# Kernel tuning notes

Hardware: AMD Instinct MI355X
Metric: run time of the kernel (lower is better)

The kernel has to match this reference:

```python
import jax, jax.numpy as jnp
import numpy as np

H = 128      # hidden_size
L = 2        # num_layers
IN0 = 96     # seq_feature_size + context_feature_size
OUT = 1

def _xavier(k, shape):
    fan_out, fan_in = shape
    lim = (6.0 / (fan_in + fan_out)) ** 0.5
    return jax.random.uniform(k, shape, jnp.float32, -lim, lim)

def _orth(k, n):
    q, _ = jnp.linalg.qr(jax.random.normal(k, (n, n)))
    return q.astype(jnp.float32)

def setup_inputs() -> dict:
    key = jax.random.key(0)
    ks = jax.random.split(key, 16)
    B, S, F_seq, F_ctx = 512, 512, 64, 32
    inp = {
        "seq_features": jax.random.normal(ks[0], (B, S, F_seq), jnp.float32),
        "context_features": jax.random.normal(ks[1], (B, F_ctx), jnp.float32),
    }
    for i in range(L):
        in_size = IN0 if i == 0 else H
        inp[f"tau{i}"] = jax.random.normal(ks[2 + 5 * i], (H,), jnp.float32) * 0.1
        inp[f"Win{i}"] = _xavier(ks[3 + 5 * i], (H, in_size))
        inp[f"Wrec{i}"] = _orth(ks[4 + 5 * i], H)
        inp[f"Wg{i}"] = _xavier(ks[5 + 5 * i], (H, in_size + H))
        inp[f"bg{i}"] = jnp.zeros((H,), jnp.float32)
    inp["W1"] = _xavier(ks[12], (H // 2, H))
    inp["b1"] = jnp.zeros((H // 2,), jnp.float32)
    inp["W2"] = _xavier(ks[13], (OUT, H // 2))
    inp["b2"] = jnp.zeros((OUT,), jnp.float32)
    return inp

def _cell_step(x, h, tau_p, Win, Wrec, Wg, bg):
    # LTC cell: RK4 integration of dh/dt = -h/tau + W_in x + gate * W_rec h
    tau = jax.nn.softplus(tau_p) + 1.0
    def rhs(hh):
        gate = jax.nn.sigmoid(jnp.tanh(jnp.concatenate([x, hh], axis=-1) @ Wg.T + bg))
        return -hh / tau + x @ Win.T + gate * (hh @ Wrec.T)
    k1 = rhs(h)
    k2 = rhs(h + 0.5 * k1)
    k3 = rhs(h + 0.5 * k2)
    k4 = rhs(h + k3)
    return jnp.tanh(h + (k1 + 2.0 * k2 + 2.0 * k3 + k4) / 6.0)

def reference(seq_features, context_features, tau0, Win0, Wrec0, Wg0, bg0,
              tau1, Win1, Wrec1, Wg1, bg1, W1, b1, W2, b2):
    B, S, _ = seq_features.shape
    ctx = jnp.broadcast_to(context_features[:, None, :], (B, S, context_features.shape[-1]))
    x = jnp.concatenate([seq_features, ctx], axis=-1)     # [B,S,IN0]
    xs = jnp.swapaxes(x, 0, 1)                            # [S,B,IN0] time-major
    cells = [(tau0, Win0, Wrec0, Wg0, bg0), (tau1, Win1, Wrec1, Wg1, bg1)]
    h_init = tuple(jnp.zeros((B, H), x.dtype) for _ in range(L))

    def step(hs, xt):
        new = []
        inp = xt
        for hi, p in zip(hs, cells):
            hn = _cell_step(inp, hi, *p)
            new.append(hn)
            inp = hn
        return tuple(new), None

    hs, _ = jax.lax.scan(step, h_init, xs)
    h_last = hs[-1]                                       # [B,H]
    # classifier (dropout is identity in eval mode)
    out = jax.nn.sigmoid(jax.nn.relu(h_last @ W1.T + b1) @ W2.T + b2)
    return out.reshape(B, -1)
```

## Files before the change

### kernel.cpp

```cpp
#include <hip/hip_runtime.h>


typedef _Float16 f16;
typedef _Float16 f16x4 __attribute__((ext_vector_type(4)));
typedef _Float16 f16x8 __attribute__((ext_vector_type(8)));
typedef float f32x4 __attribute__((ext_vector_type(4)));

#define NSTEP 512
#define OFF_A0 0
#define OFF_A1 32768
#define OFF_AIO 65536
#define OFF_AX 98304
#define W_TOTAL 122880

#define HQ0 0
#define HQ1 4352
#define L0A 8704
#define L0B 13056
#define L1A 17408
#define L1B 21760
#define L1H 26112
#define XT 30464

__device__ __forceinline__ float rcp_f(float x) { return __builtin_amdgcn_rcpf(x); }
__device__ __forceinline__ float tanh_f(float x) {
  float e = __expf(2.f * x);
  return 1.f - 2.f * rcp_f(e + 1.f);
}
__device__ __forceinline__ float sig_poly(float t) {
  float s = t * t;
  float p = fmaf(s, 2.1356861e-5f, -2.1081349e-4f);
  p = fmaf(s, p, 2.0833333e-3f);
  p = fmaf(s, p, -2.0833333e-2f);
  p = fmaf(s, p, 0.25f);
  return fmaf(t, p, 0.5f);
}

__global__ __launch_bounds__(256) void prep_kernel(
    const float* __restrict__ Win0, const float* __restrict__ Wrec0,
    const float* __restrict__ Wg0, const float* __restrict__ Win1,
    const float* __restrict__ Wrec1, const float* __restrict__ Wg1,
    f16* __restrict__ W) {
  int i = blockIdx.x * 256 + threadIdx.x;
  if (i >= W_TOTAL) return;
  if (i < OFF_AX) {
    int sec = i >> 15;
    int r = i & 32767;
    int j = r & 7, lane = (r >> 3) & 63, kc = (r >> 9) & 3, sel = (r >> 11) & 1,
        w = (r >> 12) & 7;
    int row = w * 16 + (lane & 15);
    int k = kc * 32 + ((lane >> 4) << 3) + j;
    float v;
    if (sec == 0)
      v = sel ? Wrec0[row * 128 + k] : Wg0[row * 224 + 96 + k];
    else if (sec == 1)
      v = sel ? Wrec1[row * 128 + k] : Wg1[row * 256 + 128 + k];
    else
      v = sel ? Wg1[row * 256 + k] : Win1[row * 128 + k];
    W[i] = (f16)v;
  } else {
    int r = i - OFF_AX;
    int j = r & 7, lane = (r >> 3) & 63, g = r >> 9;
    int kc = g % 3, sg = g / 3;
    int sel = sg & 1, w = sg >> 1;
    int row = w * 16 + (lane & 15);
    int k = kc * 32 + ((lane >> 4) << 3) + j;
    W[i] = (f16)(sel ? Wg0[row * 224 + k] : Win0[row * 96 + k]);
  }
}

#define MFMA16(A, B, C) __builtin_amdgcn_mfma_f32_16x16x32_f16((A), (B), (C), 0, 0, 0)
#define ZERO4 ((f32x4){0.f, 0.f, 0.f, 0.f})

#define MM2(SRC)                                                    \
  {                                                                 \
    const f16* bp_ = (SRC) + c * 136 + 8 * q;                       \
    _Pragma("unroll") for (int kc_ = 0; kc_ < 4; ++kc_) {           \
      f16x8 bf_ = *(const f16x8*)(bp_ + kc_ * 32);                  \
      ga[0] = MFMA16(awg[0][kc_], bf_, ga[0]);                      \
      ra[0] = MFMA16(awr[0][kc_], bf_, ra[0]);                      \
      ga[1] = MFMA16(awg[1][kc_], bf_, ga[1]);                      \
      ra[1] = MFMA16(awr[1][kc_], bf_, ra[1]);                      \
    }                                                               \
  }

#define MMIO(SRC, KCN)                                              \
  {                                                                 \
    const f16* bp_ = (SRC) + c * 136 + 8 * q;                       \
    _Pragma("unroll") for (int kc_ = 0; kc_ < (KCN); ++kc_) {       \
      f16x8 bf_ = *(const f16x8*)(bp_ + kc_ * 32);                  \
      ga[0] = MFMA16(au[0][kc_], bf_, ga[0]);                       \
      ra[0] = MFMA16(ag2[0][kc_], bf_, ra[0]);                      \
      ga[1] = MFMA16(au[1][kc_], bf_, ga[1]);                       \
      ra[1] = MFMA16(ag2[1][kc_], bf_, ra[1]);                      \
    }                                                               \
  }

#define GATEALL(WC, HC, DST)                                        \
  _Pragma("unroll") for (int i2_ = 0; i2_ < 2; ++i2_) {             \
    f16x4 hv_;                                                      \
    _Pragma("unroll") for (int r_ = 0; r_ < 4; ++r_) {              \
      float th_ = tanh_f(ga[i2_][r_] + gx[i2_][r_]);                \
      float gt_ = sig_poly(th_);                                    \
      float kk_ = fmaf(gt_, ra[i2_][r_],                            \
                       fmaf(-itv[i2_][r_], hhc[i2_][r_], u[i2_][r_])); \
      ksum[i2_][r_] = fmaf((WC), kk_, ksum[i2_][r_]);               \
      float hn_ = fmaf((HC), kk_, hst[i2_][r_]);                    \
      hhc[i2_][r_] = hn_;                                           \
      hv_[r_] = (f16)hn_;                                           \
    }                                                               \
    *(f16x4*)((DST) + c * 136 + jb[i2_]) = hv_;                     \
  }

#define GATEFIN(DST)                                                \
  _Pragma("unroll") for (int i2_ = 0; i2_ < 2; ++i2_) {             \
    f16x4 hv_;                                                      \
    _Pragma("unroll") for (int r_ = 0; r_ < 4; ++r_) {              \
      float th_ = tanh_f(ga[i2_][r_] + gx[i2_][r_]);                \
      float gt_ = sig_poly(th_);                                    \
      float kk_ = fmaf(gt_, ra[i2_][r_],                            \
                       fmaf(-itv[i2_][r_], hhc[i2_][r_], u[i2_][r_])); \
      float ks_ = ksum[i2_][r_] + kk_;                              \
      float hn_ = tanh_f(fmaf(ks_, 0.16666667f, hst[i2_][r_]));     \
      hst[i2_][r_] = hn_;                                           \
      hhc[i2_][r_] = hn_;                                           \
      hv_[r_] = (f16)hn_;                                           \
    }                                                               \
    *(f16x4*)((DST) + c * 136 + jb[i2_]) = hv_;                     \
  }

#define ZACC { ga[0] = ZERO4; ra[0] = ZERO4; ga[1] = ZERO4; ra[1] = ZERO4; }

__global__ __launch_bounds__(512, 2) void ltc_kernel(
    const float* __restrict__ seq, const float* __restrict__ ctx,
    const float* __restrict__ tau0p, const float* __restrict__ bg0p,
    const float* __restrict__ tau1p, const float* __restrict__ bg1p,
    const float* __restrict__ W1, const float* __restrict__ b1,
    const float* __restrict__ W2, const float* __restrict__ b2,
    const f16* __restrict__ W, float* __restrict__ out) {
  __shared__ __align__(16) char smem[32768];
  f16* hq0 = (f16*)(smem + HQ0);
  f16* hq1 = (f16*)(smem + HQ1);
  f16* l0a = (f16*)(smem + L0A);
  f16* l0b = (f16*)(smem + L0B);
  f16* l1a = (f16*)(smem + L1A);
  f16* l1b = (f16*)(smem + L1B);
  f16* l1h = (f16*)(smem + L1H);
  f16* xt = (f16*)(smem + XT);

  const int tid = threadIdx.x;
  const int w8 = tid >> 6, lane = tid & 63;
  const int q = lane >> 4, c = lane & 15;
  const int wl = w8 & 3;
  const bool isL0 = (w8 < 4);
  const int bg = blockIdx.x;
  int jb[2];
  jb[0] = 32 * wl + 4 * q;
  jb[1] = jb[0] + 16;

  f16* bufA = isL0 ? l0a : l1a;
  f16* bufB = isL0 ? l0b : l1b;

  f16x8 awg[2][4], awr[2][4], au[2][4], ag2[2][4];
  f16x8 bctx;
  if (isL0) {
#pragma unroll
    for (int i2 = 0; i2 < 2; ++i2) {
      int T = 2 * wl + i2;
#pragma unroll
      for (int kc = 0; kc < 4; ++kc) {
        awg[i2][kc] = *(const f16x8*)(W + OFF_A0 + (((T * 2 + 0) * 4 + kc) * 64 + lane) * 8);
        awr[i2][kc] = *(const f16x8*)(W + OFF_A0 + (((T * 2 + 1) * 4 + kc) * 64 + lane) * 8);
      }
#pragma unroll
      for (int kc = 0; kc < 3; ++kc) {
        au[i2][kc] = *(const f16x8*)(W + OFF_AX + (((T * 2 + 0) * 3 + kc) * 64 + lane) * 8);
        ag2[i2][kc] = *(const f16x8*)(W + OFF_AX + (((T * 2 + 1) * 3 + kc) * 64 + lane) * 8);
      }
      au[i2][3] = (f16x8)(f16)0.f;
      ag2[i2][3] = (f16x8)(f16)0.f;
    }
    const float* cp = ctx + (bg * 16 + c) * 32 + 8 * q;
#pragma unroll
    for (int j = 0; j < 8; ++j) bctx[j] = (f16)cp[j];
  } else {
#pragma unroll
    for (int i2 = 0; i2 < 2; ++i2) {
      int T = 2 * wl + i2;
#pragma unroll
      for (int kc = 0; kc < 4; ++kc) {
        awg[i2][kc] = *(const f16x8*)(W + OFF_A1 + (((T * 2 + 0) * 4 + kc) * 64 + lane) * 8);
        awr[i2][kc] = *(const f16x8*)(W + OFF_A1 + (((T * 2 + 1) * 4 + kc) * 64 + lane) * 8);
        au[i2][kc] = *(const f16x8*)(W + OFF_AIO + (((T * 2 + 0) * 4 + kc) * 64 + lane) * 8);
        ag2[i2][kc] = *(const f16x8*)(W + OFF_AIO + (((T * 2 + 1) * 4 + kc) * 64 + lane) * 8);
      }
    }
  }

  const float* taup = isL0 ? tau0p : tau1p;
  const float* bgp = isL0 ? bg0p : bg1p;
  f32x4 itv[2], bgv[2];
#pragma unroll
  for (int i2 = 0; i2 < 2; ++i2)
#pragma unroll
    for (int r = 0; r < 4; ++r) {
      float t = taup[jb[i2] + r];
      itv[i2][r] = 1.f / (logf(1.f + __expf(t)) + 1.f);
      bgv[i2][r] = bgp[jb[i2] + r];
    }

  f32x4 hst[2], hhc[2], u[2], gx[2], ksum[2], ga[2], ra[2];
  hst[0] = hst[1] = hhc[0] = hhc[1] = ZERO4;
  ksum[0] = ksum[1] = ZERO4;

  for (int j = tid; j < 2176; j += 512) {
    hq1[j] = (f16)0.f;
    l1h[j] = (f16)0.f;
  }
  const int bs = tid >> 4, fp = tid & 15;
  const size_t seqrow = ((size_t)(bg * 16 + bs)) * NSTEP * 64 + 4 * fp;
  if (tid < 256) {
    float4 sv = *(const float4*)(seq + seqrow);
    *(f16x4*)(xt + bs * 72 + 4 * fp) =
        (f16x4){(f16)sv.x, (f16)sv.y, (f16)sv.z, (f16)sv.w};
  }
  __syncthreads();

  float4 sqv = {0.f, 0.f, 0.f, 0.f};

#pragma unroll 1
  for (int i = 0; i <= NSTEP; ++i) {
    const f16* hprev = ((i + 1) & 1) ? hq1 : hq0;

    if (isL0) {
      if (i < NSTEP) {
        if (i + 1 < NSTEP) sqv = *(const float4*)(seq + seqrow + (size_t)(i + 1) * 64);
        ZACC;
        {
          f16x8 bx0 = *(const f16x8*)(xt + c * 72 + 8 * q);
          f16x8 bx1 = *(const f16x8*)(xt + c * 72 + 32 + 8 * q);
#pragma unroll
          for (int i2 = 0; i2 < 2; ++i2) {
            ga[i2] = MFMA16(au[i2][0], bx0, ga[i2]);
            ra[i2] = MFMA16(ag2[i2][0], bx0, ra[i2]);
            ga[i2] = MFMA16(au[i2][1], bx1, ga[i2]);
            ra[i2] = MFMA16(ag2[i2][1], bx1, ra[i2]);
            ga[i2] = MFMA16(au[i2][2], bctx, ga[i2]);
            ra[i2] = MFMA16(ag2[i2][2], bctx, ra[i2]);
          }
        }
#pragma unroll
        for (int i2 = 0; i2 < 2; ++i2) {
          u[i2] = ga[i2];
#pragma unroll
          for (int r = 0; r < 4; ++r) gx[i2][r] = ra[i2][r] + bgv[i2][r];
        }
        ZACC;
        MM2(hprev);
        ksum[0] = ZERO4; ksum[1] = ZERO4;
        GATEALL(1.0f, 0.5f, bufA);
      }
    } else {
      if (i >= 1) {
        ZACC;
        MMIO(hprev, 4);
#pragma unroll
        for (int i2 = 0; i2 < 2; ++i2) {
          u[i2] = ga[i2];
#pragma unroll
          for (int r = 0; r < 4; ++r) gx[i2][r] = ra[i2][r] + bgv[i2][r];
        }
        ZACC;
        MM2(l1h);
        ksum[0] = ZERO4; ksum[1] = ZERO4;
        GATEALL(1.0f, 0.5f, bufA);
      }
    }
    __syncthreads();

    if ((isL0 && i < NSTEP) || (!isL0 && i >= 1)) {
      ZACC;
      MM2(bufA);
      GATEALL(2.0f, 0.5f, bufB);
    }
    __syncthreads();

    if ((isL0 && i < NSTEP) || (!isL0 && i >= 1)) {
      ZACC;
      MM2(bufB);
      GATEALL(2.0f, 1.0f, bufA);
    }
    __syncthreads();

    if (isL0) {
      if (i < NSTEP) {
        ZACC;
        MM2(bufA);
        GATEFIN((i & 1) ? hq1 : hq0);
        if (tid < 256 && i + 1 < NSTEP)
          *(f16x4*)(xt + bs * 72 + 4 * fp) =
              (f16x4){(f16)sqv.x, (f16)sqv.y, (f16)sqv.z, (f16)sqv.w};
      }
    } else {
      if (i >= 1) {
        ZACC;
        MM2(bufA);
        GATEFIN(l1h);
      }
    }
    __syncthreads();
  }

  float* h1f = (float*)smem;
  if (!isL0) {
#pragma unroll
    for (int i2 = 0; i2 < 2; ++i2)
      *(f32x4*)(h1f + c * 132 + jb[i2]) = hst[i2];
  }
  __syncthreads();
  float* z1 = (float*)(smem + 16 * 132 * 4);
  {
    int b = tid >> 5, o = tid & 31;
#pragma unroll
    for (int hlf = 0; hlf < 2; ++hlf) {
      int oo = o + 32 * hlf;
      const float* wr = W1 + oo * 128;
      const float* hr = h1f + b * 132;
      float s = 0.f;
#pragma unroll
      for (int j = 0; j < 128; j += 4) {
        f32x4 wv = *(const f32x4*)(wr + j);
        f32x4 hv = *(const f32x4*)(hr + j);
        s += wv[0] * hv[0] + wv[1] * hv[1] + wv[2] * hv[2] + wv[3] * hv[3];
      }
      s += b1[oo];
      z1[b * 64 + oo] = fmaxf(s, 0.f);
    }
  }
  __syncthreads();
  if (tid < 16) {
    float s = b2[0];
#pragma unroll
    for (int o = 0; o < 64; ++o) s += z1[tid * 64 + o] * W2[o];
    out[bg * 16 + tid] = rcp_f(1.f + __expf(-s));
  }
}

extern "C" void kernel_launch(void* const* d_in, const int* in_sizes, int n_in,
                              void* d_out, int out_size, void* d_ws, size_t ws_size,
                              hipStream_t stream) {
  (void)in_sizes; (void)n_in; (void)out_size; (void)ws_size;
  const float* seq = (const float*)d_in[0];
  const float* ctx = (const float*)d_in[1];
  const float* tau0 = (const float*)d_in[2];
  const float* Win0 = (const float*)d_in[3];
  const float* Wrec0 = (const float*)d_in[4];
  const float* Wg0 = (const float*)d_in[5];
  const float* bg0 = (const float*)d_in[6];
  const float* tau1 = (const float*)d_in[7];
  const float* Win1 = (const float*)d_in[8];
  const float* Wrec1 = (const float*)d_in[9];
  const float* Wg1 = (const float*)d_in[10];
  const float* bg1 = (const float*)d_in[11];
  const float* W1 = (const float*)d_in[12];
  const float* b1 = (const float*)d_in[13];
  const float* W2 = (const float*)d_in[14];
  const float* b2 = (const float*)d_in[15];
  f16* W = (f16*)d_ws;

  prep_kernel<<<480, 256, 0, stream>>>(Win0, Wrec0, Wg0, Win1, Wrec1, Wg1, W);
  ltc_kernel<<<32, 512, 0, stream>>>(seq, ctx, tau0, bg0, tau1, bg1, W1, b1, W2,
                                     b2, W, (float*)d_out);
}
```

Before: 1.964 ms.

## Double-buffer input tile, precompute next-step x projection, relax barrier waits

The layer-0 input projection for step i+1 now runs during the second RK4 phase of step i, using a double-buffered x tile in shared memory, with sequence loads prefetched two steps ahead. The __syncthreads calls are replaced by an LDS-only wait plus s_barrier, so in-flight global prefetches no longer stall each barrier. The aim is to keep global-load latency and the x MFMAs off the serial recurrence path. The cost is more registers and LDS, and a heavier phase 2 for the layer-0 waves, which could shift the barrier imbalance toward them.

```diff
diff --git a/kernel.cpp b/kernel.cpp
--- a/kernel.cpp
+++ b/kernel.cpp
@@ -20,7 +20,9 @@
 #define L1A 17408
 #define L1B 21760
 #define L1H 26112
-#define XT 30464
+#define XT0 30464
+#define XT1 32768
+#define SMEM_BYTES 35072
 
 __device__ __forceinline__ float rcp_f(float x) { return __builtin_amdgcn_rcpf(x); }
 __device__ __forceinline__ float tanh_f(float x) {
@@ -35,6 +37,12 @@
   p = fmaf(s, p, 0.25f);
   return fmaf(t, p, 0.5f);
 }
+
+#define BAR()                                            \
+  do {                                                   \
+    asm volatile("s_waitcnt lgkmcnt(0)" ::: "memory");   \
+    __builtin_amdgcn_s_barrier();                        \
+  } while (0)
 
 __global__ __launch_bounds__(256) void prep_kernel(
     const float* __restrict__ Win0, const float* __restrict__ Wrec0,
@@ -96,6 +104,24 @@
     }                                                               \
   }
 
+#define XPROJ(XSRC, UD, GD)                                         \
+  {                                                                 \
+    ZACC;                                                           \
+    f16x8 bx0_ = *(const f16x8*)((XSRC) + c * 72 + 8 * q);          \
+    f16x8 bx1_ = *(const f16x8*)((XSRC) + c * 72 + 32 + 8 * q);     \
+    _Pragma("unroll") for (int i2_ = 0; i2_ < 2; ++i2_) {           \
+      ga[i2_] = MFMA16(au[i2_][0], bx0_, ga[i2_]);                  \
+      ra[i2_] = MFMA16(ag2[i2_][0], bx0_, ra[i2_]);                 \
+      ga[i2_] = MFMA16(au[i2_][1], bx1_, ga[i2_]);                  \
+      ra[i2_] = MFMA16(ag2[i2_][1], bx1_, ra[i2_]);                 \
+      ga[i2_] = MFMA16(au[i2_][2], bctx, ga[i2_]);                  \
+      ra[i2_] = MFMA16(ag2[i2_][2], bctx, ra[i2_]);                 \
+      (UD)[i2_] = ga[i2_];                                          \
+      _Pragma("unroll") for (int r_ = 0; r_ < 4; ++r_)              \
+        (GD)[i2_][r_] = ra[i2_][r_] + bgv[i2_][r_];                 \
+    }                                                               \
+  }
+
 #define GATEALL(WC, HC, DST)                                        \
   _Pragma("unroll") for (int i2_ = 0; i2_ < 2; ++i2_) {             \
     f16x4 hv_;                                                      \
@@ -138,7 +164,7 @@
     const float* __restrict__ W1, const float* __restrict__ b1,
     const float* __restrict__ W2, const float* __restrict__ b2,
     const f16* __restrict__ W, float* __restrict__ out) {
-  __shared__ __align__(16) char smem[32768];
+  __shared__ __align__(16) char smem[SMEM_BYTES];
   f16* hq0 = (f16*)(smem + HQ0);
   f16* hq1 = (f16*)(smem + HQ1);
   f16* l0a = (f16*)(smem + L0A);
@@ -146,7 +172,8 @@
   f16* l1a = (f16*)(smem + L1A);
   f16* l1b = (f16*)(smem + L1B);
   f16* l1h = (f16*)(smem + L1H);
-  f16* xt = (f16*)(smem + XT);
+  f16* xt0 = (f16*)(smem + XT0);
+  f16* xt1 = (f16*)(smem + XT1);
 
   const int tid = threadIdx.x;
   const int w8 = tid >> 6, lane = tid & 63;
@@ -210,8 +237,10 @@
     }
 
   f32x4 hst[2], hhc[2], u[2], gx[2], ksum[2], ga[2], ra[2];
+  f32x4 un[2], gxn[2];
   hst[0] = hst[1] = hhc[0] = hhc[1] = ZERO4;
   ksum[0] = ksum[1] = ZERO4;
+  un[0] = un[1] = gxn[0] = gxn[1] = ZERO4;
 
   for (int j = tid; j < 2176; j += 512) {
     hq1[j] = (f16)0.f;
@@ -219,44 +248,31 @@
   }
   const int bs = tid >> 4, fp = tid & 15;
   const size_t seqrow = ((size_t)(bg * 16 + bs)) * NSTEP * 64 + 4 * fp;
+  float4 sq_nxt = {0.f, 0.f, 0.f, 0.f};
+  float4 sq_ld = sq_nxt;
   if (tid < 256) {
     float4 sv = *(const float4*)(seq + seqrow);
-    *(f16x4*)(xt + bs * 72 + 4 * fp) =
+    *(f16x4*)(xt0 + bs * 72 + 4 * fp) =
         (f16x4){(f16)sv.x, (f16)sv.y, (f16)sv.z, (f16)sv.w};
+    sq_nxt = *(const float4*)(seq + seqrow + 64);
   }
   __syncthreads();
-
-  float4 sqv = {0.f, 0.f, 0.f, 0.f};
+  if (isL0) { XPROJ(xt0, u, gx); }
 
 #pragma unroll 1
   for (int i = 0; i <= NSTEP; ++i) {
     const f16* hprev = ((i + 1) & 1) ? hq1 : hq0;
+    f16* xw = ((i + 1) & 1) ? xt1 : xt0;
 
     if (isL0) {
       if (i < NSTEP) {
-        if (i + 1 < NSTEP) sqv = *(const float4*)(seq + seqrow + (size_t)(i + 1) * 64);
-        ZACC;
-        {
-          f16x8 bx0 = *(const f16x8*)(xt + c * 72 + 8 * q);
-          f16x8 bx1 = *(const f16x8*)(xt + c * 72 + 32 + 8 * q);
-#pragma unroll
-          for (int i2 = 0; i2 < 2; ++i2) {
-            ga[i2] = MFMA16(au[i2][0], bx0, ga[i2]);
-            ra[i2] = MFMA16(ag2[i2][0], bx0, ra[i2]);
-            ga[i2] = MFMA16(au[i2][1], bx1, ga[i2]);
-            ra[i2] = MFMA16(ag2[i2][1], bx1, ra[i2]);
-            ga[i2] = MFMA16(au[i2][2], bctx, ga[i2]);
-            ra[i2] = MFMA16(ag2[i2][2], bctx, ra[i2]);
-          }
-        }
-#pragma unroll
-        for (int i2 = 0; i2 < 2; ++i2) {
-          u[i2] = ga[i2];
-#pragma unroll
-          for (int r = 0; r < 4; ++r) gx[i2][r] = ra[i2][r] + bgv[i2][r];
-        }
+        if (i + 2 < NSTEP)
+          sq_ld = *(const float4*)(seq + seqrow + (size_t)(i + 2) * 64);
         ZACC;
         MM2(hprev);
+        if (i + 1 < NSTEP)
+          *(f16x4*)(xw + bs * 72 + 4 * fp) =
+              (f16x4){(f16)sq_nxt.x, (f16)sq_nxt.y, (f16)sq_nxt.z, (f16)sq_nxt.w};
         ksum[0] = ZERO4; ksum[1] = ZERO4;
         GATEALL(1.0f, 0.5f, bufA);
       }
@@ -276,39 +292,46 @@
         GATEALL(1.0f, 0.5f, bufA);
       }
     }
-    __syncthreads();
-
-    if ((isL0 && i < NSTEP) || (!isL0 && i >= 1)) {
+    BAR();
+
+    if (isL0) {
+      if (i < NSTEP) {
+        ZACC;
+        MM2(bufA);
+        GATEALL(2.0f, 0.5f, bufB);
+        if (i + 1 < NSTEP) { XPROJ(xw, un, gxn); }
+      }
+    } else if (i >= 1) {
       ZACC;
       MM2(bufA);
       GATEALL(2.0f, 0.5f, bufB);
     }
-    __syncthreads();
+    BAR();
 
     if ((isL0 && i < NSTEP) || (!isL0 && i >= 1)) {
       ZACC;
       MM2(bufB);
       GATEALL(2.0f, 1.0f, bufA);
     }
-    __syncthreads();
+    BAR();
 
     if (isL0) {
       if (i < NSTEP) {
         ZACC;
         MM2(bufA);
         GATEFIN((i & 1) ? hq1 : hq0);
-        if (tid < 256 && i + 1 < NSTEP)
-          *(f16x4*)(xt + bs * 72 + 4 * fp) =
-              (f16x4){(f16)sqv.x, (f16)sqv.y, (f16)sqv.z, (f16)sqv.w};
-      }
-    } else {
-      if (i >= 1) {
-        ZACC;
-        MM2(bufA);
-        GATEFIN(l1h);
-      }
-    }
-    __syncthreads();
+        if (i + 1 < NSTEP) {
+          u[0] = un[0]; u[1] = un[1];
+          gx[0] = gxn[0]; gx[1] = gxn[1];
+          if (i + 2 < NSTEP) sq_nxt = sq_ld;
+        }
+      }
+    } else if (i >= 1) {
+      ZACC;
+      MM2(bufA);
+      GATEFIN(l1h);
+    }
+    BAR();
   }
 
   float* h1f = (float*)smem;
```

Result: no change. 1.926 ms (-1.9%).
